# Optimization experiments

Hardware: AMD Instinct MI355X
Metric: run time of the kernel (lower is better)

The kernel has to match this reference:

```python
import jax, jax.numpy as jnp
import numpy as np

EPS_MAG = 1e-6    # magnitude threshold for valid trajectory
EPS_WSUM = 1e-8   # clamp on combined weight sum


def setup_inputs() -> dict:
    key = jax.random.key(0)
    embeddings = jax.random.normal(key, (4, 4096, 1024), dtype=jnp.float32)
    return {"embeddings": embeddings, "max_trajectory_distance": 8}


def reference(embeddings, max_trajectory_distance):
    # Vectorized form of compute_sparse_trajectories:
    # for each pos p >= 1, window of diffs d[start..p-1], start = max(0, p - max_dist),
    # normalized diffs weighted by linspace(0.1, 1.0, window) * tanh(2*|d|),
    # output[p] = weighted sum / clamp(weight sum, 1e-8); output[0] = 0.
    B, S, D = embeddings.shape
    maxd = min(int(max_trajectory_distance), S - 1)

    d = embeddings[:, 1:, :] - embeddings[:, :-1, :]            # [B, S-1, D]
    mag = jnp.linalg.norm(d, axis=-1)                           # [B, S-1]
    normed = jnp.where((mag > EPS_MAG)[..., None],
                       d / jnp.maximum(mag, EPS_MAG)[..., None],
                       0.0)                                     # [B, S-1, D]
    magw = jnp.tanh(mag * 2.0)                                  # [B, S-1]

    p = jnp.arange(S)                                           # positions
    wsize = jnp.minimum(maxd, p)                                # window size per pos
    j = jnp.arange(maxd)
    idx = p[:, None] - maxd + j[None, :]                        # [S, maxd] diff indices (end-aligned)
    valid = idx >= 0                                            # [S, maxd]
    # k = rank within window (0..wsize-1): weights linspace(0.1, 1.0, wsize)
    k = (j[None, :] - (maxd - wsize)[:, None]).astype(jnp.float32)
    denom = jnp.maximum(wsize - 1, 1).astype(jnp.float32)[:, None]
    lin = jnp.where(wsize[:, None] > 1, 0.1 + 0.9 * k / denom, 0.1)
    lin = jnp.where(valid, lin, 0.0)                            # [S, maxd]

    ci = jnp.clip(idx, 0, S - 2)                                # safe gather indices
    n_g = normed[:, ci, :]                                      # [B, S, maxd, D]
    m_g = magw[:, ci]                                           # [B, S, maxd]
    comb = lin[None, :, :] * m_g * valid[None, :, :]            # combined weights

    wsum = jnp.maximum(comb.sum(axis=-1), EPS_WSUM)             # [B, S]
    traj = jnp.einsum('bsjd,bsj->bsd', n_g, comb) / wsum[..., None]
    return traj
```

## Files before the change

kernel.cpp:

```cpp
#include <hip/hip_runtime.h>
#include <hip/hip_bf16.h>


constexpr int B_ = 4;
constexpr int S_ = 4096;
constexpr int D_ = 1024;
constexpr int MAXD  = 8;
constexpr int CHUNK = 32;
constexpr int ROWS  = CHUNK + MAXD;
constexpr int NDIFF = ROWS - 1;
constexpr int NCH   = S_ / CHUNK;
constexpr int NWG   = B_ * NCH;
constexpr int NXCD  = 8;

__global__ __launch_bounds__(512, 4)
void traj_splat_kernel(const float* __restrict__ emb, float* __restrict__ out) {
    const int bid = blockIdx.x;
    const int lin = (bid % NXCD) * (NWG / NXCD) + bid / NXCD;
    const int schunk = lin & (NCH - 1);
    const int b      = lin >> 7;

    const int s0   = schunk * CHUNK;
    const int lane = threadIdx.x & 63;
    const int wave = threadIdx.x >> 6;
    const int d0   = threadIdx.x * 2;

    const float* __restrict__ embB = emb + (size_t)b * S_ * D_;

    __shared__ float part[NDIFF][33];
    __shared__ float smagw[NDIFF];
    __shared__ float sq[NDIFF];
    __shared__ float gco[CHUNK][12];

    float2 win[ROWS];
    #pragma unroll
    for (int r = 0; r < ROWS; ++r) {
        const int row = s0 - MAXD + r;
        win[r] = (row >= 0) ? *(const float2*)(embB + (size_t)row * D_ + d0)
                            : make_float2(0.f, 0.f);
    }

    #pragma unroll
    for (int li = 0; li < NDIFF; ++li) {
        const float2 a = win[li], c = win[li + 1];
        const float dx = c.x - a.x, dy = c.y - a.y;
        float sum = dx * dx + dy * dy;
        sum += __shfl_xor(sum, 32, 64);
        sum += __shfl_xor(sum, 16, 64);
        sum += __shfl_xor(sum,  8, 64);
        sum += __shfl_xor(sum,  4, 64);
        if (lane < 4) part[li][wave * 4 + lane] = sum;
    }
    __syncthreads();

    if (threadIdx.x < NDIFF) {
        const int li = threadIdx.x;
        float s2 = 0.f;
        #pragma unroll
        for (int k = 0; k < 32; ++k) s2 += part[li][k];
        const float mag = sqrtf(s2);
        const float mw  = tanhf(2.f * mag);
        smagw[li] = mw;
        sq[li]    = (mag > 1e-6f) ? (mw / mag) : 0.f;
    }
    __syncthreads();

    if (threadIdx.x < CHUNK) {
        const int sl = threadIdx.x;
        const int s  = s0 + sl;
        const int ws = min(MAXD, s);
        const int lo = MAXD - ws;
        const float rden = 0.9f / (float)max(ws - 1, 1);

        float cpad[MAXD + 2];
        #pragma unroll
        for (int t = 0; t < MAXD + 2; ++t) cpad[t] = 0.f;

        float wsum = 0.f;
        #pragma unroll
        for (int j = 0; j < MAXD; ++j) {
            if (j >= lo) {
                const int li = sl + j;
                const float lin2 = (ws > 1) ? (0.1f + rden * (float)(j - lo)) : 0.1f;
                wsum += lin2 * smagw[li];
                cpad[j + 1] = lin2 * sq[li];
            }
        }
        const float inv = 1.f / fmaxf(wsum, 1e-8f);
        #pragma unroll
        for (int jr = 0; jr <= MAXD; ++jr)
            gco[sl][jr] = (cpad[jr] - cpad[jr + 1]) * inv;
    }
    __syncthreads();

    float* outB = out + ((size_t)b * S_ + s0) * D_ + d0;
    #pragma unroll
    for (int sl = 0; sl < CHUNK; ++sl) {
        const float4 g0 = *(const float4*)&gco[sl][0];
        const float4 g1 = *(const float4*)&gco[sl][4];
        const float  g8 = gco[sl][8];

        float2 acc;
        acc.x = g0.x * win[sl].x;
        acc.y = g0.x * win[sl].y;
        const float gs[8] = {g0.y, g0.z, g0.w, g1.x, g1.y, g1.z, g1.w, g8};
        #pragma unroll
        for (int jr = 1; jr <= MAXD; ++jr) {
            const float g = gs[jr - 1];
            acc.x += g * win[sl + jr].x;
            acc.y += g * win[sl + jr].y;
        }
        *(float2*)(outB + (size_t)sl * D_) = acc;
    }
}

extern "C" void kernel_launch(void* const* d_in, const int* in_sizes, int n_in,
                              void* d_out, int out_size, void* d_ws, size_t ws_size,
                              hipStream_t stream) {
    const float* emb = (const float*)d_in[0];
    float* out = (float*)d_out;

    dim3 grid(NWG);
    dim3 block(512);
    traj_splat_kernel<<<grid, block, 0, stream>>>(emb, out);
}
```

Baseline: 29.23 us.

## Process four sub-chunks per workgroup with register prefetch of next rows

Each workgroup now covers 64 sequence positions in four sub-chunks of 16, sliding a register window and prefetching the next 16 rows while the current sub-chunk is reduced and written. This removes the 8-row halo reload per 32-row chunk and overlaps global loads with compute. Barriers become raw s_barrier with an lgkmcnt wait, and occupancy drops to 2 workgroups per CU with fewer workgroups overall. The risks are higher register pressure and less parallelism, since the grid halves.

```diff
diff --git a/kernel.cpp b/kernel.cpp
--- a/kernel.cpp
+++ b/kernel.cpp
@@ -5,112 +5,144 @@
 constexpr int B_ = 4;
 constexpr int S_ = 4096;
 constexpr int D_ = 1024;
-constexpr int MAXD  = 8;
-constexpr int CHUNK = 32;
-constexpr int ROWS  = CHUNK + MAXD;
-constexpr int NDIFF = ROWS - 1;
-constexpr int NCH   = S_ / CHUNK;
+constexpr int MAXD = 8;
+constexpr int SUB   = 16;
+constexpr int NSUB  = 4;
+constexpr int SPAN  = SUB * NSUB;
+constexpr int WIN   = SUB + MAXD;
+constexpr int NDIF0 = WIN - 1;
+constexpr int NCH   = S_ / SPAN;
 constexpr int NWG   = B_ * NCH;
 constexpr int NXCD  = 8;
 
-__global__ __launch_bounds__(512, 4)
+__device__ __forceinline__ void lds_barrier() {
+    asm volatile("s_waitcnt lgkmcnt(0)" ::: "memory");
+    __builtin_amdgcn_s_barrier();
+}
+
+__global__ __launch_bounds__(512, 2)
 void traj_splat_kernel(const float* __restrict__ emb, float* __restrict__ out) {
     const int bid = blockIdx.x;
     const int lin = (bid % NXCD) * (NWG / NXCD) + bid / NXCD;
-    const int schunk = lin & (NCH - 1);
-    const int b      = lin >> 7;
+    const int sc  = lin & (NCH - 1);
+    const int b   = lin >> 6;
 
-    const int s0   = schunk * CHUNK;
+    const int s0b  = sc * SPAN;
     const int lane = threadIdx.x & 63;
     const int wave = threadIdx.x >> 6;
     const int d0   = threadIdx.x * 2;
 
     const float* __restrict__ embB = emb + (size_t)b * S_ * D_;
+    float* __restrict__ outB = out + (size_t)b * S_ * D_;
 
-    __shared__ float part[NDIFF][33];
-    __shared__ float smagw[NDIFF];
-    __shared__ float sq[NDIFF];
-    __shared__ float gco[CHUNK][12];
+    __shared__ float part[NDIF0][33];
+    __shared__ float smagw[SPAN + MAXD];
+    __shared__ float sq[SPAN + MAXD];
+    __shared__ float gco[SUB][12];
 
-    float2 win[ROWS];
+    float2 win[WIN];
+    float2 nxt[SUB];
+
     #pragma unroll
-    for (int r = 0; r < ROWS; ++r) {
-        const int row = s0 - MAXD + r;
+    for (int r = 0; r < WIN; ++r) {
+        const int row = s0b - MAXD + r;
         win[r] = (row >= 0) ? *(const float2*)(embB + (size_t)row * D_ + d0)
                             : make_float2(0.f, 0.f);
     }
 
     #pragma unroll
-    for (int li = 0; li < NDIFF; ++li) {
-        const float2 a = win[li], c = win[li + 1];
-        const float dx = c.x - a.x, dy = c.y - a.y;
-        float sum = dx * dx + dy * dy;
-        sum += __shfl_xor(sum, 32, 64);
-        sum += __shfl_xor(sum, 16, 64);
-        sum += __shfl_xor(sum,  8, 64);
-        sum += __shfl_xor(sum,  4, 64);
-        if (lane < 4) part[li][wave * 4 + lane] = sum;
-    }
-    __syncthreads();
+    for (int j = 0; j < NSUB; ++j) {
+        const int r0 = s0b + j * SUB;
 
-    if (threadIdx.x < NDIFF) {
-        const int li = threadIdx.x;
-        float s2 = 0.f;
+        if (j + 1 < NSUB) {
+            #pragma unroll
+            for (int t = 0; t < SUB; ++t)
+                nxt[t] = *(const float2*)(embB + (size_t)(r0 + SUB + t) * D_ + d0);
+        }
+
+        const int ndiff = (j == 0) ? NDIF0 : SUB;
+        const int woff  = (j == 0) ? 0 : (MAXD - 1);
+        const int dbase = (j == 0) ? 0 : (16 * j + 7);
         #pragma unroll
-        for (int k = 0; k < 32; ++k) s2 += part[li][k];
-        const float mag = sqrtf(s2);
-        const float mw  = tanhf(2.f * mag);
-        smagw[li] = mw;
-        sq[li]    = (mag > 1e-6f) ? (mw / mag) : 0.f;
-    }
-    __syncthreads();
-
-    if (threadIdx.x < CHUNK) {
-        const int sl = threadIdx.x;
-        const int s  = s0 + sl;
-        const int ws = min(MAXD, s);
-        const int lo = MAXD - ws;
-        const float rden = 0.9f / (float)max(ws - 1, 1);
-
-        float cpad[MAXD + 2];
-        #pragma unroll
-        for (int t = 0; t < MAXD + 2; ++t) cpad[t] = 0.f;
-
-        float wsum = 0.f;
-        #pragma unroll
-        for (int j = 0; j < MAXD; ++j) {
-            if (j >= lo) {
-                const int li = sl + j;
-                const float lin2 = (ws > 1) ? (0.1f + rden * (float)(j - lo)) : 0.1f;
-                wsum += lin2 * smagw[li];
-                cpad[j + 1] = lin2 * sq[li];
+        for (int t = 0; t < NDIF0; ++t) {
+            if (t < ndiff) {
+                const float2 a = win[t + woff], c = win[t + woff + 1];
+                const float dx = c.x - a.x, dy = c.y - a.y;
+                float sum = dx * dx + dy * dy;
+                sum += __shfl_xor(sum, 32, 64);
+                sum += __shfl_xor(sum, 16, 64);
+                sum += __shfl_xor(sum,  8, 64);
+                sum += __shfl_xor(sum,  4, 64);
+                if (lane < 4) part[t][wave * 4 + lane] = sum;
             }
         }
-        const float inv = 1.f / fmaxf(wsum, 1e-8f);
+        lds_barrier();
+
+        if ((int)threadIdx.x < ndiff) {
+            const int t = threadIdx.x;
+            float s2 = 0.f;
+            #pragma unroll
+            for (int k = 0; k < 32; ++k) s2 += part[t][k];
+            const float mag = sqrtf(s2);
+            const float mw  = tanhf(2.f * mag);
+            smagw[dbase + t] = mw;
+            sq[dbase + t]    = (mag > 1e-6f) ? (mw / mag) : 0.f;
+        }
+        lds_barrier();
+
+        if (threadIdx.x < SUB) {
+            const int sl = threadIdx.x;
+            const int s  = r0 + sl;
+            const int ws = min(MAXD, s);
+            const int lo = MAXD - ws;
+            const float rden = 0.9f / (float)max(ws - 1, 1);
+
+            float cpad[MAXD + 2];
+            #pragma unroll
+            for (int t = 0; t < MAXD + 2; ++t) cpad[t] = 0.f;
+
+            float wsum = 0.f;
+            #pragma unroll
+            for (int jj = 0; jj < MAXD; ++jj) {
+                if (jj >= lo) {
+                    const int di = 16 * j + sl + jj;
+                    const float lin2 = (ws > 1) ? (0.1f + rden * (float)(jj - lo)) : 0.1f;
+                    wsum += lin2 * smagw[di];
+                    cpad[jj + 1] = lin2 * sq[di];
+                }
+            }
+            const float inv = 1.f / fmaxf(wsum, 1e-8f);
+            #pragma unroll
+            for (int jr = 0; jr <= MAXD; ++jr)
+                gco[sl][jr] = (cpad[jr] - cpad[jr + 1]) * inv;
+        }
+        lds_barrier();
+
+        float* op = outB + (size_t)r0 * D_ + d0;
         #pragma unroll
-        for (int jr = 0; jr <= MAXD; ++jr)
-            gco[sl][jr] = (cpad[jr] - cpad[jr + 1]) * inv;
-    }
-    __syncthreads();
+        for (int sl = 0; sl < SUB; ++sl) {
+            const float4 g0 = *(const float4*)&gco[sl][0];
+            const float4 g1 = *(const float4*)&gco[sl][4];
+            const float  g8 = gco[sl][8];
 
-    float* outB = out + ((size_t)b * S_ + s0) * D_ + d0;
-    #pragma unroll
-    for (int sl = 0; sl < CHUNK; ++sl) {
-        const float4 g0 = *(const float4*)&gco[sl][0];
-        const float4 g1 = *(const float4*)&gco[sl][4];
-        const float  g8 = gco[sl][8];
+            float2 acc;
+            acc.x = g0.x * win[sl].x;
+            acc.y = g0.x * win[sl].y;
+            const float gs[8] = {g0.y, g0.z, g0.w, g1.x, g1.y, g1.z, g1.w, g8};
+            #pragma unroll
+            for (int jr = 1; jr <= MAXD; ++jr) {
+                acc.x += gs[jr - 1] * win[sl + jr].x;
+                acc.y += gs[jr - 1] * win[sl + jr].y;
+            }
+            *(float2*)(op + (size_t)sl * D_) = acc;
+        }
 
-        float2 acc;
-        acc.x = g0.x * win[sl].x;
-        acc.y = g0.x * win[sl].y;
-        const float gs[8] = {g0.y, g0.z, g0.w, g1.x, g1.y, g1.z, g1.w, g8};
-        #pragma unroll
-        for (int jr = 1; jr <= MAXD; ++jr) {
-            const float g = gs[jr - 1];
-            acc.x += g * win[sl + jr].x;
-            acc.y += g * win[sl + jr].y;
+        if (j + 1 < NSUB) {
+            #pragma unroll
+            for (int t = 0; t < MAXD; ++t) win[t] = win[t + SUB];
+            #pragma unroll
+            for (int t = 0; t < SUB; ++t) win[MAXD + t] = nxt[t];
         }
-        *(float2*)(outB + (size_t)sl * D_) = acc;
     }
 }
 
```

Result: slower. 37.85 us (+29.5%).
